# Kernel optimization log

Hardware: AMD Instinct MI355X
Metric: run time of the kernel (lower is better)

Reference implementation:

```python
import jax, jax.numpy as jnp
import numpy as np

D_IN = 2048
NUM_HEADS = 16
QK_NOPE = 64
QK_ROPE = 64
QK_HEAD = QK_NOPE + QK_ROPE  # 128
V_HEAD = 128
KV_LORA = 1024
SEQ = 4096
BATCH = 1
SCALE = QK_HEAD ** -0.5
EPS = 1e-6


def rmsnorm(x, w):
    return x * jax.lax.rsqrt(jnp.mean(x * x, axis=-1, keepdims=True) + EPS) * w


def apply_rope(x, cos, sin):
    # x: [B, S, H, D]; cos/sin: [S, D//2]; pairs are consecutive elements (view_as_complex)
    b, s, h, d = x.shape
    xr = x.reshape(b, s, h, d // 2, 2)
    xe, xo = xr[..., 0], xr[..., 1]
    c = cos[None, :, None, :]
    sn = sin[None, :, None, :]
    oe = xe * c - xo * sn
    oo = xe * sn + xo * c
    return jnp.stack([oe, oo], axis=-1).reshape(b, s, h, d)


def setup_inputs() -> dict:
    key = jax.random.key(0)
    ks = jax.random.split(key, 8)
    x = jax.random.normal(ks[0], (BATCH, SEQ, D_IN), dtype=jnp.float32)
    # rotary tables (rope_theta=10000)
    inv_freq = 1.0 / (10000.0 ** (np.arange(0, QK_ROPE, 2, dtype=np.float32) / QK_ROPE))
    angles = np.arange(SEQ, dtype=np.float32)[:, None] * inv_freq[None, :]
    cos = jnp.asarray(np.cos(angles), dtype=jnp.float32)
    sin = jnp.asarray(np.sin(angles), dtype=jnp.float32)
    # causal additive mask [S, S]
    mask = jnp.where(jnp.triu(jnp.ones((SEQ, SEQ), dtype=bool), k=1), -1e9, 0.0).astype(jnp.float32)
    def lin(k, fan_out, fan_in):
        bound = 1.0 / np.sqrt(fan_in)
        return jax.random.uniform(k, (fan_out, fan_in), jnp.float32, -bound, bound)
    wq = lin(ks[1], NUM_HEADS * QK_HEAD, D_IN)
    wkv_a = lin(ks[2], KV_LORA + QK_ROPE, D_IN)
    kv_norm_w = jnp.ones((KV_LORA,), dtype=jnp.float32)
    wkv_b = lin(ks[3], NUM_HEADS * (QK_NOPE + V_HEAD), KV_LORA)
    wo = lin(ks[4], D_IN, NUM_HEADS * V_HEAD)
    return {"x": x, "cos": cos, "sin": sin, "mask": mask, "wq": wq,
            "wkv_a": wkv_a, "kv_norm_w": kv_norm_w, "wkv_b": wkv_b, "wo": wo,
            "start_pos": 0}


def reference(x, cos, sin, mask, wq, wkv_a, kv_norm_w, wkv_b, wo, start_pos):
    b, s, _ = x.shape
    # Q projection -> [B, S, H, qk_head_dim]
    q = (x @ wq.T).reshape(b, s, NUM_HEADS, QK_HEAD)
    q_nope, q_pe = q[..., :QK_NOPE], q[..., QK_NOPE:]
    q_pe = apply_rope(q_pe, cos, sin)
    # KV low-rank projection
    kv_full = x @ wkv_a.T                               # [B, S, KV_LORA + QK_ROPE]
    kv, k_pe = kv_full[..., :KV_LORA], kv_full[..., KV_LORA:]
    k_pe = apply_rope(k_pe[:, :, None, :], cos, sin)    # [B, S, 1, QK_ROPE]
    # naive path: expand latent to per-head k_nope / v
    q = jnp.concatenate([q_nope, q_pe], axis=-1)        # [B, S, H, 128]
    kvb = (rmsnorm(kv, kv_norm_w) @ wkv_b.T).reshape(b, s, NUM_HEADS, QK_NOPE + V_HEAD)
    k_nope, v = kvb[..., :QK_NOPE], kvb[..., QK_NOPE:]
    k = jnp.concatenate([k_nope, jnp.broadcast_to(k_pe, (b, s, NUM_HEADS, QK_ROPE))], axis=-1)
    # start_pos=0 prefill: cache[:, :end_pos] == freshly written k, v
    scores = jnp.einsum('bqhd,bkhd->bqhk', q, k) * SCALE  # [B, S, H, S]
    scores = scores + mask[None, :, None, :]
    probs = jax.nn.softmax(scores.astype(jnp.float32), axis=-1).astype(x.dtype)
    out = jnp.einsum('bqhk,bkhd->bqhd', probs, v)       # [B, S, H, V_HEAD]
    return out.reshape(b, s, NUM_HEADS * V_HEAD) @ wo.T
```

## Files before the change

kernel.cpp:

```cpp
#include <hip/hip_runtime.h>

typedef __bf16 bf16;
typedef __attribute__((ext_vector_type(8))) __bf16 bf16x8;
typedef __attribute__((ext_vector_type(2))) __bf16 bf16x2;
typedef __attribute__((ext_vector_type(4))) float f32x4;
typedef __attribute__((ext_vector_type(4))) int int4v;

typedef __attribute__((address_space(1))) const void gconst_t;
typedef __attribute__((address_space(3))) void lvoid_t;

#define SEQ 4096
#define D_IN 2048
#define NHEADS 16
#define QSCALE (0.08838834764831843f * 1.4426950408889634f)
#define RMS_EPS 1e-6f
#define QKV_N 3136

__device__ inline unsigned pack2bf(float a, float b) {
    bf16x2 t; t[0] = (bf16)a; t[1] = (bf16)b;
    return __builtin_bit_cast(unsigned, t);
}

__device__ inline void conv_seg(const float* __restrict__ in, bf16* __restrict__ out,
                                int n, int i0, int stride) {
    for (int i = i0; i < n; i += stride) {
        float4 v = *reinterpret_cast<const float4*>(in + i);
        bf16 o[4];
        o[0] = (bf16)v.x; o[1] = (bf16)v.y; o[2] = (bf16)v.z; o[3] = (bf16)v.w;
        *reinterpret_cast<uint2*>(out + i) = *reinterpret_cast<uint2*>(o);
    }
}

__global__ __launch_bounds__(256) void convert_all_kernel(
    const float* __restrict__ xs,  const float* __restrict__ wqs,
    const float* __restrict__ was, const float* __restrict__ wbs,
    const float* __restrict__ wos,
    bf16* __restrict__ xd, bf16* __restrict__ wqd, bf16* __restrict__ wad,
    bf16* __restrict__ wbd, bf16* __restrict__ wod) {
    int i0 = (blockIdx.x * 256 + threadIdx.x) * 4;
    int stride = gridDim.x * 256 * 4;
    conv_seg(xs,  xd,  4096 * 2048, i0, stride);
    conv_seg(wqs, wqd, 2048 * 2048, i0, stride);
    conv_seg(was, wad, 1088 * 2048, i0, stride);
    conv_seg(wbs, wbd, 3072 * 1024, i0, stride);
    conv_seg(wos, wod, 2048 * 2048, i0, stride);
}

template<int BN, bool BF16_OUT>
__global__ __launch_bounds__(512, 2) void gemm256_kernel(
    const bf16* __restrict__ A, const bf16* __restrict__ B, void* __restrict__ Cout,
    int M, int N, int K) {
    constexpr int CB = BN / 64;
    constexpr int NF = BN / 64;
    constexpr int WC = BN / 4;
    __shared__ __align__(16) bf16 Al[2][256 * 64];
    __shared__ __align__(16) bf16 Bl[2][BN * 64];

    int t    = threadIdx.x;
    int lane = t & 63;
    int w    = t >> 6;
    int wr   = w >> 2;
    int wc   = w & 3;
    int l15  = lane & 15;
    int g    = lane >> 4;
    int m0 = blockIdx.y * 256;
    int n0 = blockIdx.x * BN;

    f32x4 acc[8][NF] = {};

    auto stage = [&](int kt, int buf) {
        int k0 = kt << 6;
        #pragma unroll
        for (int c = 0; c < 4; c++) {
            int idx = c * 512 + t;
            int r = idx >> 3;
            int u = (idx & 7) ^ (r & 7);
            const bf16* ga = A + (size_t)(m0 + r) * K + k0 + u * 8;
            __builtin_amdgcn_global_load_lds((gconst_t*)ga,
                (lvoid_t*)&Al[buf][(c * 512 + w * 64) * 8], 16, 0, 0);
        }
        #pragma unroll
        for (int c = 0; c < CB; c++) {
            int idx = c * 512 + t;
            int r = idx >> 3;
            int u = (idx & 7) ^ (r & 7);
            int br = n0 + r; if (br >= N) br = N - 1;
            const bf16* gb = B + (size_t)br * K + k0 + u * 8;
            __builtin_amdgcn_global_load_lds((gconst_t*)gb,
                (lvoid_t*)&Bl[buf][(c * 512 + w * 64) * 8], 16, 0, 0);
        }
    };

    int nt = K >> 6;
    stage(0, 0);
    for (int kt = 0; kt < nt; ++kt) {
        int buf = kt & 1;
        if (kt + 1 < nt) {
            stage(kt + 1, buf ^ 1);
            __builtin_amdgcn_sched_barrier(0);
            if constexpr (BN == 256) asm volatile("s_waitcnt vmcnt(8)" ::: "memory");
            else                     asm volatile("s_waitcnt vmcnt(6)" ::: "memory");
            __builtin_amdgcn_sched_barrier(0);
        } else {
            __builtin_amdgcn_sched_barrier(0);
            asm volatile("s_waitcnt vmcnt(0)" ::: "memory");
            __builtin_amdgcn_sched_barrier(0);
        }
        __builtin_amdgcn_s_barrier();

        #pragma unroll
        for (int ks = 0; ks < 2; ++ks) {
            bf16x8 af[8], bfv[NF];
            #pragma unroll
            for (int mt = 0; mt < 8; mt++) {
                int ra = wr * 128 + mt * 16 + l15;
                int u = (ks * 4 + g) ^ (ra & 7);
                af[mt] = *reinterpret_cast<const bf16x8*>(&Al[buf][ra * 64 + u * 8]);
            }
            #pragma unroll
            for (int nf = 0; nf < NF; nf++) {
                int rb = wc * WC + nf * 16 + l15;
                int u = (ks * 4 + g) ^ (rb & 7);
                bfv[nf] = *reinterpret_cast<const bf16x8*>(&Bl[buf][rb * 64 + u * 8]);
            }
            __builtin_amdgcn_s_setprio(1);
            #pragma unroll
            for (int mt = 0; mt < 8; mt++)
                #pragma unroll
                for (int nf = 0; nf < NF; nf++)
                    acc[mt][nf] = __builtin_amdgcn_mfma_f32_16x16x32_bf16(af[mt], bfv[nf], acc[mt][nf], 0, 0, 0);
            __builtin_amdgcn_s_setprio(0);
        }
        __builtin_amdgcn_s_barrier();
    }

    #pragma unroll
    for (int mt = 0; mt < 8; mt++) {
        #pragma unroll
        for (int nf = 0; nf < NF; nf++) {
            int col = n0 + wc * WC + nf * 16 + l15;
            if (col < N) {
                #pragma unroll
                for (int r = 0; r < 4; r++) {
                    int row = m0 + wr * 128 + mt * 16 + g * 4 + r;
                    if (BF16_OUT)
                        ((bf16*)Cout)[(size_t)row * N + col] = (bf16)acc[mt][nf][r];
                    else
                        ((float*)Cout)[(size_t)row * N + col] = acc[mt][nf][r];
                }
            }
        }
    }
}

__global__ __launch_bounds__(256) void prep_qkv_kernel(
    bf16* __restrict__ qkv, const float* __restrict__ w,
    const float* __restrict__ cosb, const float* __restrict__ sinb,
    bf16* __restrict__ kvnorm, bf16* __restrict__ kpe) {
    __shared__ float red[4];
    int s = blockIdx.x;
    int t = threadIdx.x;

    const bf16* src = qkv + (size_t)s * QKV_N + 2048;
    float f[4];
    {
        uint2 raw = *reinterpret_cast<const uint2*>(src + t * 4);
        bf16* vb = reinterpret_cast<bf16*>(&raw);
        float ss = 0.f;
        #pragma unroll
        for (int j = 0; j < 4; j++) { f[j] = (float)vb[j]; ss += f[j] * f[j]; }
        #pragma unroll
        for (int m = 1; m < 64; m <<= 1) ss += __shfl_xor(ss, m);
        if ((t & 63) == 0) red[t >> 6] = ss;
    }
    __syncthreads();
    float tot = red[0] + red[1] + red[2] + red[3];
    float rms = rsqrtf(tot * (1.0f / 1024.0f) + RMS_EPS);
    bf16 o[4];
    #pragma unroll
    for (int j = 0; j < 4; j++) o[j] = (bf16)(f[j] * rms * w[t*4 + j]);
    *reinterpret_cast<uint2*>(kvnorm + (size_t)s * 1024 + t * 4) = *reinterpret_cast<uint2*>(o);
    if (t < 16) {
        float e[4];
        #pragma unroll
        for (int j = 0; j < 4; j++) e[j] = (float)src[1024 + t*4 + j];
        int ib = t * 2;
        float c0 = cosb[s*32 + ib],     s0 = sinb[s*32 + ib];
        float c1 = cosb[s*32 + ib + 1], s1 = sinb[s*32 + ib + 1];
        bf16 ko[4];
        ko[0] = (bf16)(e[0]*c0 - e[1]*s0);
        ko[1] = (bf16)(e[0]*s0 + e[1]*c0);
        ko[2] = (bf16)(e[2]*c1 - e[3]*s1);
        ko[3] = (bf16)(e[2]*s1 + e[3]*c1);
        *reinterpret_cast<uint2*>(kpe + (size_t)s * 64 + t * 4) = *reinterpret_cast<uint2*>(ko);
    }

    bf16* p = qkv + (size_t)s * QKV_N + t * 8;
    bf16x8 v = *reinterpret_cast<bf16x8*>(p);
    float qf[8];
    #pragma unroll
    for (int j = 0; j < 8; j++) qf[j] = (float)v[j];
    int d0 = (t & 15) * 8;
    if (d0 >= 64) {
        int ib = (d0 - 64) >> 1;
        #pragma unroll
        for (int pr = 0; pr < 4; pr++) {
            float c  = cosb[s * 32 + ib + pr];
            float sn = sinb[s * 32 + ib + pr];
            float xe = qf[pr*2], xo = qf[pr*2 + 1];
            qf[pr*2]     = xe * c - xo * sn;
            qf[pr*2 + 1] = xe * sn + xo * c;
        }
    }
    #pragma unroll
    for (int j = 0; j < 8; j++) v[j] = (bf16)(qf[j] * QSCALE);
    *reinterpret_cast<bf16x8*>(p) = v;
}

__global__ __launch_bounds__(256) void build_vt_kernel(
    const bf16* __restrict__ kvb, bf16* __restrict__ vt) {
    const int LT = 130;
    __shared__ bf16 lt[64 * 130];
    int h  = blockIdx.y;
    int s0 = blockIdx.x * 64;
    int t  = threadIdx.x;
    {
        int row = t >> 2;
        int d0  = (t & 3) * 32;
        const bf16* src = kvb + (size_t)(s0 + row) * 3072 + h * 192 + 64 + d0;
        int4v v0 = *reinterpret_cast<const int4v*>(src);
        int4v v1 = *reinterpret_cast<const int4v*>(src + 8);
        int4v v2 = *reinterpret_cast<const int4v*>(src + 16);
        int4v v3 = *reinterpret_cast<const int4v*>(src + 24);
        int* dst = reinterpret_cast<int*>(&lt[row * LT + d0]);
        int* s0p = reinterpret_cast<int*>(&v0); int* s1p = reinterpret_cast<int*>(&v1);
        int* s2p = reinterpret_cast<int*>(&v2); int* s3p = reinterpret_cast<int*>(&v3);
        #pragma unroll
        for (int j = 0; j < 4; j++) { dst[j] = s0p[j]; dst[4+j] = s1p[j]; dst[8+j] = s2p[j]; dst[12+j] = s3p[j]; }
    }
    __syncthreads();
    int ss = t & 63;
    int db = t >> 6;
    bf16* out = vt + (size_t)h * 128 * 4096 + s0 + ss;
    #pragma unroll
    for (int dd = db; dd < 128; dd += 4)
        out[(size_t)dd * 4096] = lt[ss * LT + dd];
}

__global__ __launch_bounds__(256, 2) void attn_kernel(
    const bf16* __restrict__ q,
    const bf16* __restrict__ kvb,
    const bf16* __restrict__ kpe,
    const bf16* __restrict__ vt,
    bf16* __restrict__ attn) {
    const int LPS = 72;
    __shared__ __align__(16) bf16 Kl[2][64 * 128];
    __shared__ __align__(16) bf16 Vl[2][128 * 64];
    __shared__ __align__(16) bf16 Pl[4][16 * 72];
    __shared__ __align__(16) float bcast[4][16];

    int h    = blockIdx.y;
    int tile = (h < 8) ? (31 - (int)blockIdx.x) : (int)blockIdx.x;
    int q0   = tile * 128;
    int t  = threadIdx.x;
    int lane = t & 63;
    int w  = t >> 6;
    int l15 = lane & 15;
    int g   = lane >> 4;
    int sw  = l15 & 7;
    int qrow = q0 + w * 32;

    const bf16* kvbh = kvb + h * 192;
    const bf16* vth  = vt + (size_t)h * 524288;

    bf16x8 qf[2][4];
    #pragma unroll
    for (int mt = 0; mt < 2; mt++) {
        const bf16* qp = q + (size_t)(qrow + mt*16 + l15) * QKV_N + h * 128 + g * 8;
        #pragma unroll
        for (int c = 0; c < 4; c++) qf[mt][c] = *reinterpret_cast<const bf16x8*>(qp + c * 32);
    }

    f32x4 o[2][8] = {};
    float mrow[2], lrow[2];
    #pragma unroll
    for (int mt = 0; mt < 2; mt++) { mrow[mt] = -3e38f; lrow[mt] = 0.f; }

    int nch = (q0 >> 6) + 2;
    int dc  = (q0 >> 6) + (w >> 1);

    auto stageK = [&](int jc, int buf) {
        int j0 = jc << 6;
        #pragma unroll
        for (int c = 0; c < 4; c++) {
            int idx = c*256 + w*64 + lane;
            int row = idx >> 4;
            int u   = (idx & 15) ^ (row & 7);
            const bf16* src = (u < 8)
                ? kvbh + (size_t)(j0 + row) * 3072 + u * 8
                : kpe  + (size_t)(j0 + row) * 64  + (u - 8) * 8;
            __builtin_amdgcn_global_load_lds((gconst_t*)src,
                (lvoid_t*)&Kl[buf][(c*256 + w*64) * 8], 16, 0, 0);
        }
    };
    auto stageV = [&](int jc, int buf) {
        int j0 = jc << 6;
        #pragma unroll
        for (int c = 0; c < 4; c++) {
            int idx = c*256 + w*64 + lane;
            int row = idx >> 3;
            int u   = (idx & 7) ^ (row & 7);
            const bf16* src = vth + (size_t)row * 4096 + j0 + u * 8;
            __builtin_amdgcn_global_load_lds((gconst_t*)src,
                (lvoid_t*)&Vl[buf][(c*256 + w*64) * 8], 16, 0, 0);
        }
    };

    stageK(0, 0); stageV(0, 0);

    for (int jc = 0; jc < nch; ++jc) {
        __syncthreads();
        if (jc + 1 < nch) { stageK(jc + 1, (jc + 1) & 1); stageV(jc + 1, (jc + 1) & 1); }

        if (jc <= dc) {
            int cur = jc & 1;
            int j0  = jc << 6;
            bool masked = (jc == dc);

            f32x4 sfr[2][4];
            #pragma unroll
            for (int s = 0; s < 4; ++s) {
                int krow = s*16 + l15;
                bf16x8 kf[4];
                #pragma unroll
                for (int c = 0; c < 4; ++c)
                    kf[c] = *reinterpret_cast<const bf16x8*>(
                        &Kl[cur][krow*128 + (((c*4 + g) ^ sw) * 8)]);
                #pragma unroll
                for (int mt = 0; mt < 2; ++mt) {
                    f32x4 acc = {};
                    acc = __builtin_amdgcn_mfma_f32_16x16x32_bf16(kf[0], qf[mt][0], acc, 0, 0, 0);
                    acc = __builtin_amdgcn_mfma_f32_16x16x32_bf16(kf[1], qf[mt][1], acc, 0, 0, 0);
                    acc = __builtin_amdgcn_mfma_f32_16x16x32_bf16(kf[2], qf[mt][2], acc, 0, 0, 0);
                    acc = __builtin_amdgcn_mfma_f32_16x16x32_bf16(kf[3], qf[mt][3], acc, 0, 0, 0);
                    sfr[mt][s] = acc;
                }
            }

            bf16x8 pf[2][2];
            #pragma unroll
            for (int mt = 0; mt < 2; ++mt) {
                int i = qrow + mt*16 + l15;
                if (masked) {
                    #pragma unroll
                    for (int s = 0; s < 4; ++s)
                        #pragma unroll
                        for (int r = 0; r < 4; ++r) {
                            int j = j0 + s*16 + g*4 + r;
                            if (j > i) sfr[mt][s][r] = -3e38f;
                        }
                }
                float m01 = fmaxf(fmaxf(sfr[mt][0][0], sfr[mt][0][1]),
                                  fmaxf(sfr[mt][0][2], sfr[mt][0][3]));
                float m23 = fmaxf(fmaxf(sfr[mt][1][0], sfr[mt][1][1]),
                                  fmaxf(sfr[mt][1][2], sfr[mt][1][3]));
                float m45 = fmaxf(fmaxf(sfr[mt][2][0], sfr[mt][2][1]),
                                  fmaxf(sfr[mt][2][2], sfr[mt][2][3]));
                float m67 = fmaxf(fmaxf(sfr[mt][3][0], sfr[mt][3][1]),
                                  fmaxf(sfr[mt][3][2], sfr[mt][3][3]));
                float mloc = fmaxf(fmaxf(m01, m23), fmaxf(m45, m67));
                float mx = fmaxf(mloc, __shfl_xor(mloc, 16));
                mx = fmaxf(mx, __shfl_xor(mx, 32));
                bool need = mx > mrow[mt];
                float mnew = fmaxf(mrow[mt], mx);
                float sfac = __builtin_amdgcn_exp2f(mrow[mt] - mnew);
                mrow[mt] = mnew;
                float psum = 0.f;
                #pragma unroll
                for (int s = 0; s < 4; ++s)
                    #pragma unroll
                    for (int r = 0; r < 4; ++r) {
                        float p = __builtin_amdgcn_exp2f(sfr[mt][s][r] - mnew);
                        sfr[mt][s][r] = p;
                        psum += p;
                    }
                lrow[mt] = lrow[mt] * sfac + psum;
                #pragma unroll
                for (int s = 0; s < 4; ++s) {
                    unsigned u0 = pack2bf(sfr[mt][s][0], sfr[mt][s][1]);
                    unsigned u1 = pack2bf(sfr[mt][s][2], sfr[mt][s][3]);
                    *reinterpret_cast<unsigned*>(&Pl[w][l15 * LPS + s*16 + g*4])     = u0;
                    *reinterpret_cast<unsigned*>(&Pl[w][l15 * LPS + s*16 + g*4 + 2]) = u1;
                }
                if (g == 0) bcast[w][l15] = sfac;
                f32x4 sf4 = *reinterpret_cast<const f32x4*>(&bcast[w][g*4]);
                if (__any(need)) {
                    #pragma unroll
                    for (int dt = 0; dt < 8; ++dt)
                        #pragma unroll
                        for (int r = 0; r < 4; ++r) o[mt][dt][r] *= sf4[r];
                }
                pf[mt][0] = *reinterpret_cast<const bf16x8*>(&Pl[w][l15 * LPS + g * 8]);
                pf[mt][1] = *reinterpret_cast<const bf16x8*>(&Pl[w][l15 * LPS + 32 + g * 8]);
            }

            #pragma unroll
            for (int dt = 0; dt < 8; ++dt) {
                int vrow = dt*16 + l15;
                bf16x8 va = *reinterpret_cast<const bf16x8*>(
                    &Vl[cur][vrow*64 + ((g ^ sw) * 8)]);
                bf16x8 vb = *reinterpret_cast<const bf16x8*>(
                    &Vl[cur][vrow*64 + (((4 + g) ^ sw) * 8)]);
                o[0][dt] = __builtin_amdgcn_mfma_f32_16x16x32_bf16(pf[0][0], va, o[0][dt], 0, 0, 0);
                o[0][dt] = __builtin_amdgcn_mfma_f32_16x16x32_bf16(pf[0][1], vb, o[0][dt], 0, 0, 0);
                o[1][dt] = __builtin_amdgcn_mfma_f32_16x16x32_bf16(pf[1][0], va, o[1][dt], 0, 0, 0);
                o[1][dt] = __builtin_amdgcn_mfma_f32_16x16x32_bf16(pf[1][1], vb, o[1][dt], 0, 0, 0);
            }
        }
    }

    #pragma unroll
    for (int mt = 0; mt < 2; ++mt) {
        float l = lrow[mt];
        l += __shfl_xor(l, 16);
        l += __shfl_xor(l, 32);
        float linv = __builtin_amdgcn_rcpf(l);
        if (g == 0) bcast[w][l15] = linv;
        f32x4 li4 = *reinterpret_cast<const f32x4*>(&bcast[w][g*4]);
        #pragma unroll
        for (int r = 0; r < 4; ++r) {
            int i = qrow + mt*16 + g*4 + r;
            #pragma unroll
            for (int dt = 0; dt < 8; ++dt)
                attn[(size_t)i * 2048 + h * 128 + dt*16 + l15] = (bf16)(o[mt][dt][r] * li4[r]);
        }
    }
}

extern "C" void kernel_launch(void* const* d_in, const int* in_sizes, int n_in,
                              void* d_out, int out_size, void* d_ws, size_t ws_size,
                              hipStream_t stream) {
    const float* x    = (const float*)d_in[0];
    const float* cosb = (const float*)d_in[1];
    const float* sinb = (const float*)d_in[2];
    const float* wq   = (const float*)d_in[4];
    const float* wkva = (const float*)d_in[5];
    const float* kvw  = (const float*)d_in[6];
    const float* wkvb = (const float*)d_in[7];
    const float* wo   = (const float*)d_in[8];

    char* ws = (char*)d_ws;
    bf16* x_bf    = (bf16*)(ws + 0);
    bf16* kvnorm  = (bf16*)(ws + 0);
    bf16* attn    = (bf16*)(ws + 0);
    bf16* wq_bf   = (bf16*)(ws + 16777216);
    bf16* wkva_bf = (bf16*)(ws + 25165824);
    bf16* wkvb_bf = (bf16*)(ws + 29622272);
    bf16* wo_bf   = (bf16*)(ws + 35913728);
    bf16* qkv     = (bf16*)(ws + 44302336);
    bf16* kpe     = (bf16*)(ws + 69992448);
    bf16* kvb     = (bf16*)(ws + 70516736);
    bf16* vt      = (bf16*)(ws + 95682560);

    convert_all_kernel<<<dim3(2048), dim3(256), 0, stream>>>(
        x, wq, wkva, wkvb, wo, x_bf, wq_bf, wkva_bf, wkvb_bf, wo_bf);

    gemm256_kernel<256, true><<<dim3(13, 16), dim3(512), 0, stream>>>(x_bf, wq_bf, qkv, 4096, QKV_N, 2048);

    prep_qkv_kernel<<<dim3(4096), dim3(256), 0, stream>>>(qkv, kvw, cosb, sinb, kvnorm, kpe);

    gemm256_kernel<256, true><<<dim3(12, 16), dim3(512), 0, stream>>>(kvnorm, wkvb_bf, kvb, 4096, 3072, 1024);

    build_vt_kernel<<<dim3(64, 16), dim3(256), 0, stream>>>(kvb, vt);

    attn_kernel<<<dim3(32, 16), dim3(256), 0, stream>>>(qkv, kvb, kpe, vt, attn);

    gemm256_kernel<128, false><<<dim3(16, 16), dim3(512), 0, stream>>>(attn, wo_bf, (float*)d_out, 4096, 2048, 2048);
}
```

Measured before the change: 327.7 us.

## Shrink attention query tile to 64 rows and drop K/V double buffering

The attention kernel now handles 64 query rows per block (16 per wave) instead of 128, launches twice as many blocks, and uses single-buffered K/V shared memory with load-then-sync instead of a prefetched double buffer. Occupancy rises to 3 blocks per CU thanks to the smaller LDS and register footprint. The aim is more parallelism and better load balance across the causal triangle. In exchange, each K/V chunk is loaded twice as often per query row, there is no overlap between loads and compute inside a block, and MFMA reuse of each K fragment is halved.

```diff
diff --git a/kernel.cpp b/kernel.cpp
--- a/kernel.cpp
+++ b/kernel.cpp
@@ -247,49 +247,45 @@
         out[(size_t)dd * 4096] = lt[ss * LT + dd];
 }
 
-__global__ __launch_bounds__(256, 2) void attn_kernel(
+__global__ __launch_bounds__(256, 3) void attn_kernel(
     const bf16* __restrict__ q,
     const bf16* __restrict__ kvb,
     const bf16* __restrict__ kpe,
     const bf16* __restrict__ vt,
     bf16* __restrict__ attn) {
     const int LPS = 72;
-    __shared__ __align__(16) bf16 Kl[2][64 * 128];
-    __shared__ __align__(16) bf16 Vl[2][128 * 64];
+    __shared__ __align__(16) bf16 Kl[64 * 128];
+    __shared__ __align__(16) bf16 Vl[128 * 64];
     __shared__ __align__(16) bf16 Pl[4][16 * 72];
     __shared__ __align__(16) float bcast[4][16];
 
     int h    = blockIdx.y;
-    int tile = (h < 8) ? (31 - (int)blockIdx.x) : (int)blockIdx.x;
-    int q0   = tile * 128;
+    int tile = 63 - (int)blockIdx.x;
+    int q0   = tile * 64;
     int t  = threadIdx.x;
     int lane = t & 63;
     int w  = t >> 6;
     int l15 = lane & 15;
     int g   = lane >> 4;
     int sw  = l15 & 7;
-    int qrow = q0 + w * 32;
+    int qrow = q0 + w * 16;
 
     const bf16* kvbh = kvb + h * 192;
     const bf16* vth  = vt + (size_t)h * 524288;
 
-    bf16x8 qf[2][4];
-    #pragma unroll
-    for (int mt = 0; mt < 2; mt++) {
-        const bf16* qp = q + (size_t)(qrow + mt*16 + l15) * QKV_N + h * 128 + g * 8;
-        #pragma unroll
-        for (int c = 0; c < 4; c++) qf[mt][c] = *reinterpret_cast<const bf16x8*>(qp + c * 32);
-    }
-
-    f32x4 o[2][8] = {};
-    float mrow[2], lrow[2];
-    #pragma unroll
-    for (int mt = 0; mt < 2; mt++) { mrow[mt] = -3e38f; lrow[mt] = 0.f; }
-
-    int nch = (q0 >> 6) + 2;
-    int dc  = (q0 >> 6) + (w >> 1);
-
-    auto stageK = [&](int jc, int buf) {
+    bf16x8 qf[4];
+    {
+        const bf16* qp = q + (size_t)(qrow + l15) * QKV_N + h * 128 + g * 8;
+        #pragma unroll
+        for (int c = 0; c < 4; c++) qf[c] = *reinterpret_cast<const bf16x8*>(qp + c * 32);
+    }
+
+    f32x4 o[8] = {};
+    float mrow = -3e38f, lrow = 0.f;
+
+    int nch = tile + 1;
+
+    auto stageK = [&](int jc) {
         int j0 = jc << 6;
         #pragma unroll
         for (int c = 0; c < 4; c++) {
@@ -300,10 +296,10 @@
                 ? kvbh + (size_t)(j0 + row) * 3072 + u * 8
                 : kpe  + (size_t)(j0 + row) * 64  + (u - 8) * 8;
             __builtin_amdgcn_global_load_lds((gconst_t*)src,
-                (lvoid_t*)&Kl[buf][(c*256 + w*64) * 8], 16, 0, 0);
+                (lvoid_t*)&Kl[(c*256 + w*64) * 8], 16, 0, 0);
         }
     };
-    auto stageV = [&](int jc, int buf) {
+    auto stageV = [&](int jc) {
         int j0 = jc << 6;
         #pragma unroll
         for (int c = 0; c < 4; c++) {
@@ -312,116 +308,97 @@
             int u   = (idx & 7) ^ (row & 7);
             const bf16* src = vth + (size_t)row * 4096 + j0 + u * 8;
             __builtin_amdgcn_global_load_lds((gconst_t*)src,
-                (lvoid_t*)&Vl[buf][(c*256 + w*64) * 8], 16, 0, 0);
+                (lvoid_t*)&Vl[(c*256 + w*64) * 8], 16, 0, 0);
         }
     };
 
-    stageK(0, 0); stageV(0, 0);
-
     for (int jc = 0; jc < nch; ++jc) {
+        stageK(jc); stageV(jc);
         __syncthreads();
-        if (jc + 1 < nch) { stageK(jc + 1, (jc + 1) & 1); stageV(jc + 1, (jc + 1) & 1); }
-
-        if (jc <= dc) {
-            int cur = jc & 1;
-            int j0  = jc << 6;
-            bool masked = (jc == dc);
-
-            f32x4 sfr[2][4];
-            #pragma unroll
-            for (int s = 0; s < 4; ++s) {
-                int krow = s*16 + l15;
-                bf16x8 kf[4];
+        int j0 = jc << 6;
+        bool masked = (jc == tile);
+
+        f32x4 sfr[4];
+        #pragma unroll
+        for (int s = 0; s < 4; ++s) {
+            int krow = s*16 + l15;
+            bf16x8 kf[4];
+            #pragma unroll
+            for (int c = 0; c < 4; ++c)
+                kf[c] = *reinterpret_cast<const bf16x8*>(
+                    &Kl[krow*128 + (((c*4 + g) ^ sw) * 8)]);
+            f32x4 acc = {};
+            acc = __builtin_amdgcn_mfma_f32_16x16x32_bf16(kf[0], qf[0], acc, 0, 0, 0);
+            acc = __builtin_amdgcn_mfma_f32_16x16x32_bf16(kf[1], qf[1], acc, 0, 0, 0);
+            acc = __builtin_amdgcn_mfma_f32_16x16x32_bf16(kf[2], qf[2], acc, 0, 0, 0);
+            acc = __builtin_amdgcn_mfma_f32_16x16x32_bf16(kf[3], qf[3], acc, 0, 0, 0);
+            sfr[s] = acc;
+        }
+
+        int i = qrow + l15;
+        if (masked) {
+            #pragma unroll
+            for (int s = 0; s < 4; ++s)
                 #pragma unroll
-                for (int c = 0; c < 4; ++c)
-                    kf[c] = *reinterpret_cast<const bf16x8*>(
-                        &Kl[cur][krow*128 + (((c*4 + g) ^ sw) * 8)]);
+                for (int r = 0; r < 4; ++r) {
+                    int j = j0 + s*16 + g*4 + r;
+                    if (j > i) sfr[s][r] = -3e38f;
+                }
+        }
+        float m01 = fmaxf(fmaxf(sfr[0][0], sfr[0][1]), fmaxf(sfr[0][2], sfr[0][3]));
+        float m23 = fmaxf(fmaxf(sfr[1][0], sfr[1][1]), fmaxf(sfr[1][2], sfr[1][3]));
+        float m45 = fmaxf(fmaxf(sfr[2][0], sfr[2][1]), fmaxf(sfr[2][2], sfr[2][3]));
+        float m67 = fmaxf(fmaxf(sfr[3][0], sfr[3][1]), fmaxf(sfr[3][2], sfr[3][3]));
+        float mloc = fmaxf(fmaxf(m01, m23), fmaxf(m45, m67));
+        float mx = fmaxf(mloc, __shfl_xor(mloc, 16));
+        mx = fmaxf(mx, __shfl_xor(mx, 32));
+        bool need = mx > mrow;
+        float mnew = fmaxf(mrow, mx);
+        float sfac = __builtin_amdgcn_exp2f(mrow - mnew);
+        mrow = mnew;
+        float psum = 0.f;
+        #pragma unroll
+        for (int s = 0; s < 4; ++s)
+            #pragma unroll
+            for (int r = 0; r < 4; ++r) {
+                float p = __builtin_amdgcn_exp2f(sfr[s][r] - mnew);
+                sfr[s][r] = p;
+                psum += p;
+            }
+        lrow = lrow * sfac + psum;
+        #pragma unroll
+        for (int s = 0; s < 4; ++s) {
+            unsigned u0 = pack2bf(sfr[s][0], sfr[s][1]);
+            unsigned u1 = pack2bf(sfr[s][2], sfr[s][3]);
+            *reinterpret_cast<unsigned*>(&Pl[w][l15 * LPS + s*16 + g*4])     = u0;
+            *reinterpret_cast<unsigned*>(&Pl[w][l15 * LPS + s*16 + g*4 + 2]) = u1;
+        }
+        if (g == 0) bcast[w][l15] = sfac;
+        f32x4 sf4 = *reinterpret_cast<const f32x4*>(&bcast[w][g*4]);
+        if (__any(need)) {
+            #pragma unroll
+            for (int dt = 0; dt < 8; ++dt)
                 #pragma unroll
-                for (int mt = 0; mt < 2; ++mt) {
-                    f32x4 acc = {};
-                    acc = __builtin_amdgcn_mfma_f32_16x16x32_bf16(kf[0], qf[mt][0], acc, 0, 0, 0);
-                    acc = __builtin_amdgcn_mfma_f32_16x16x32_bf16(kf[1], qf[mt][1], acc, 0, 0, 0);
-                    acc = __builtin_amdgcn_mfma_f32_16x16x32_bf16(kf[2], qf[mt][2], acc, 0, 0, 0);
-                    acc = __builtin_amdgcn_mfma_f32_16x16x32_bf16(kf[3], qf[mt][3], acc, 0, 0, 0);
-                    sfr[mt][s] = acc;
-                }
-            }
-
-            bf16x8 pf[2][2];
-            #pragma unroll
-            for (int mt = 0; mt < 2; ++mt) {
-                int i = qrow + mt*16 + l15;
-                if (masked) {
-                    #pragma unroll
-                    for (int s = 0; s < 4; ++s)
-                        #pragma unroll
-                        for (int r = 0; r < 4; ++r) {
-                            int j = j0 + s*16 + g*4 + r;
-                            if (j > i) sfr[mt][s][r] = -3e38f;
-                        }
-                }
-                float m01 = fmaxf(fmaxf(sfr[mt][0][0], sfr[mt][0][1]),
-                                  fmaxf(sfr[mt][0][2], sfr[mt][0][3]));
-                float m23 = fmaxf(fmaxf(sfr[mt][1][0], sfr[mt][1][1]),
-                                  fmaxf(sfr[mt][1][2], sfr[mt][1][3]));
-                float m45 = fmaxf(fmaxf(sfr[mt][2][0], sfr[mt][2][1]),
-                                  fmaxf(sfr[mt][2][2], sfr[mt][2][3]));
-                float m67 = fmaxf(fmaxf(sfr[mt][3][0], sfr[mt][3][1]),
-                                  fmaxf(sfr[mt][3][2], sfr[mt][3][3]));
-                float mloc = fmaxf(fmaxf(m01, m23), fmaxf(m45, m67));
-                float mx = fmaxf(mloc, __shfl_xor(mloc, 16));
-                mx = fmaxf(mx, __shfl_xor(mx, 32));
-                bool need = mx > mrow[mt];
-                float mnew = fmaxf(mrow[mt], mx);
-                float sfac = __builtin_amdgcn_exp2f(mrow[mt] - mnew);
-                mrow[mt] = mnew;
-                float psum = 0.f;
-                #pragma unroll
-                for (int s = 0; s < 4; ++s)
-                    #pragma unroll
-                    for (int r = 0; r < 4; ++r) {
-                        float p = __builtin_amdgcn_exp2f(sfr[mt][s][r] - mnew);
-                        sfr[mt][s][r] = p;
-                        psum += p;
-                    }
-                lrow[mt] = lrow[mt] * sfac + psum;
-                #pragma unroll
-                for (int s = 0; s < 4; ++s) {
-                    unsigned u0 = pack2bf(sfr[mt][s][0], sfr[mt][s][1]);
-                    unsigned u1 = pack2bf(sfr[mt][s][2], sfr[mt][s][3]);
-                    *reinterpret_cast<unsigned*>(&Pl[w][l15 * LPS + s*16 + g*4])     = u0;
-                    *reinterpret_cast<unsigned*>(&Pl[w][l15 * LPS + s*16 + g*4 + 2]) = u1;
-                }
-                if (g == 0) bcast[w][l15] = sfac;
-                f32x4 sf4 = *reinterpret_cast<const f32x4*>(&bcast[w][g*4]);
-                if (__any(need)) {
-                    #pragma unroll
-                    for (int dt = 0; dt < 8; ++dt)
-                        #pragma unroll
-                        for (int r = 0; r < 4; ++r) o[mt][dt][r] *= sf4[r];
-                }
-                pf[mt][0] = *reinterpret_cast<const bf16x8*>(&Pl[w][l15 * LPS + g * 8]);
-                pf[mt][1] = *reinterpret_cast<const bf16x8*>(&Pl[w][l15 * LPS + 32 + g * 8]);
-            }
-
-            #pragma unroll
-            for (int dt = 0; dt < 8; ++dt) {
-                int vrow = dt*16 + l15;
-                bf16x8 va = *reinterpret_cast<const bf16x8*>(
-                    &Vl[cur][vrow*64 + ((g ^ sw) * 8)]);
-                bf16x8 vb = *reinterpret_cast<const bf16x8*>(
-                    &Vl[cur][vrow*64 + (((4 + g) ^ sw) * 8)]);
-                o[0][dt] = __builtin_amdgcn_mfma_f32_16x16x32_bf16(pf[0][0], va, o[0][dt], 0, 0, 0);
-                o[0][dt] = __builtin_amdgcn_mfma_f32_16x16x32_bf16(pf[0][1], vb, o[0][dt], 0, 0, 0);
-                o[1][dt] = __builtin_amdgcn_mfma_f32_16x16x32_bf16(pf[1][0], va, o[1][dt], 0, 0, 0);
-                o[1][dt] = __builtin_amdgcn_mfma_f32_16x16x32_bf16(pf[1][1], vb, o[1][dt], 0, 0, 0);
-            }
-        }
-    }
-
-    #pragma unroll
-    for (int mt = 0; mt < 2; ++mt) {
-        float l = lrow[mt];
+                for (int r = 0; r < 4; ++r) o[dt][r] *= sf4[r];
+        }
+        bf16x8 pf0 = *reinterpret_cast<const bf16x8*>(&Pl[w][l15 * LPS + g * 8]);
+        bf16x8 pf1 = *reinterpret_cast<const bf16x8*>(&Pl[w][l15 * LPS + 32 + g * 8]);
+
+        #pragma unroll
+        for (int dt = 0; dt < 8; ++dt) {
+            int vrow = dt*16 + l15;
+            bf16x8 va = *reinterpret_cast<const bf16x8*>(
+                &Vl[vrow*64 + ((g ^ sw) * 8)]);
+            bf16x8 vb = *reinterpret_cast<const bf16x8*>(
+                &Vl[vrow*64 + (((4 + g) ^ sw) * 8)]);
+            o[dt] = __builtin_amdgcn_mfma_f32_16x16x32_bf16(pf0, va, o[dt], 0, 0, 0);
+            o[dt] = __builtin_amdgcn_mfma_f32_16x16x32_bf16(pf1, vb, o[dt], 0, 0, 0);
+        }
+        __syncthreads();
+    }
+
+    {
+        float l = lrow;
         l += __shfl_xor(l, 16);
         l += __shfl_xor(l, 32);
         float linv = __builtin_amdgcn_rcpf(l);
@@ -429,10 +406,10 @@
         f32x4 li4 = *reinterpret_cast<const f32x4*>(&bcast[w][g*4]);
         #pragma unroll
         for (int r = 0; r < 4; ++r) {
-            int i = qrow + mt*16 + g*4 + r;
+            int i = qrow + g*4 + r;
             #pragma unroll
             for (int dt = 0; dt < 8; ++dt)
-                attn[(size_t)i * 2048 + h * 128 + dt*16 + l15] = (bf16)(o[mt][dt][r] * li4[r]);
+                attn[(size_t)i * 2048 + h * 128 + dt*16 + l15] = (bf16)(o[dt][r] * li4[r]);
         }
     }
 }
@@ -473,7 +450,7 @@
 
     build_vt_kernel<<<dim3(64, 16), dim3(256), 0, stream>>>(kvb, vt);
 
-    attn_kernel<<<dim3(32, 16), dim3(256), 0, stream>>>(qkv, kvb, kpe, vt, attn);
+    attn_kernel<<<dim3(64, 16), dim3(256), 0, stream>>>(qkv, kvb, kpe, vt, attn);
 
     gemm256_kernel<128, false><<<dim3(16, 16), dim3(512), 0, stream>>>(attn, wo_bf, (float*)d_out, 4096, 2048, 2048);
 }
```

Measured after the change: 371.6 us. +13.4%, slower.

## Interleave next-tile global-to-LDS loads across four compute phases in GEMM

Applied to the files above, without the earlier changes.

The GEMM K-loop is split into four phases, each covering half a K-step and half the M rows. The global_load_lds prefetches for the next tile are spread across these phases instead of being issued all at once, so memory traffic overlaps MFMA work more evenly. Only four A fragments are held at a time, which lowers register pressure. In exchange there are more workgroup barriers per K tile, and a tighter vmcnt wait at phase 0.

```diff
diff --git a/kernel.cpp b/kernel.cpp
--- a/kernel.cpp
+++ b/kernel.cpp
@@ -68,70 +68,75 @@
 
     f32x4 acc[8][NF] = {};
 
-    auto stage = [&](int kt, int buf) {
-        int k0 = kt << 6;
-        #pragma unroll
-        for (int c = 0; c < 4; c++) {
-            int idx = c * 512 + t;
-            int r = idx >> 3;
-            int u = (idx & 7) ^ (r & 7);
-            const bf16* ga = A + (size_t)(m0 + r) * K + k0 + u * 8;
-            __builtin_amdgcn_global_load_lds((gconst_t*)ga,
-                (lvoid_t*)&Al[buf][(c * 512 + w * 64) * 8], 16, 0, 0);
-        }
-        #pragma unroll
-        for (int c = 0; c < CB; c++) {
-            int idx = c * 512 + t;
-            int r = idx >> 3;
-            int u = (idx & 7) ^ (r & 7);
-            int br = n0 + r; if (br >= N) br = N - 1;
-            const bf16* gb = B + (size_t)br * K + k0 + u * 8;
-            __builtin_amdgcn_global_load_lds((gconst_t*)gb,
-                (lvoid_t*)&Bl[buf][(c * 512 + w * 64) * 8], 16, 0, 0);
-        }
+    auto stageA = [&](int kt2, int buf2, int c) {
+        int k0 = kt2 << 6;
+        int idx = c * 512 + t;
+        int r = idx >> 3;
+        int u = (idx & 7) ^ (r & 7);
+        const bf16* ga = A + (size_t)(m0 + r) * K + k0 + u * 8;
+        __builtin_amdgcn_global_load_lds((gconst_t*)ga,
+            (lvoid_t*)&Al[buf2][(c * 512 + w * 64) * 8], 16, 0, 0);
     };
+    auto stageB = [&](int kt2, int buf2, int c) {
+        int k0 = kt2 << 6;
+        int idx = c * 512 + t;
+        int r = idx >> 3;
+        int u = (idx & 7) ^ (r & 7);
+        int br = n0 + r; if (br >= N) br = N - 1;
+        const bf16* gb = B + (size_t)br * K + k0 + u * 8;
+        __builtin_amdgcn_global_load_lds((gconst_t*)gb,
+            (lvoid_t*)&Bl[buf2][(c * 512 + w * 64) * 8], 16, 0, 0);
+    };
 
     int nt = K >> 6;
-    stage(0, 0);
+    #pragma unroll
+    for (int c = 0; c < 4; c++)  stageA(0, 0, c);
+    #pragma unroll
+    for (int c = 0; c < CB; c++) stageB(0, 0, c);
+
     for (int kt = 0; kt < nt; ++kt) {
         int buf = kt & 1;
-        if (kt + 1 < nt) {
-            stage(kt + 1, buf ^ 1);
-            __builtin_amdgcn_sched_barrier(0);
-            if constexpr (BN == 256) asm volatile("s_waitcnt vmcnt(8)" ::: "memory");
-            else                     asm volatile("s_waitcnt vmcnt(6)" ::: "memory");
-            __builtin_amdgcn_sched_barrier(0);
-        } else {
-            __builtin_amdgcn_sched_barrier(0);
-            asm volatile("s_waitcnt vmcnt(0)" ::: "memory");
-            __builtin_amdgcn_sched_barrier(0);
-        }
-        __builtin_amdgcn_s_barrier();
-
-        #pragma unroll
-        for (int ks = 0; ks < 2; ++ks) {
-            bf16x8 af[8], bfv[NF];
-            #pragma unroll
-            for (int mt = 0; mt < 8; mt++) {
-                int ra = wr * 128 + mt * 16 + l15;
+        bool has_next = (kt + 1 < nt);
+        bf16x8 bfv[NF];
+        #pragma unroll
+        for (int ph = 0; ph < 4; ++ph) {
+            int ks = ph >> 1, mh = ph & 1;
+            if (has_next) {
+                stageA(kt + 1, buf ^ 1, ph);
+                if (ph < CB) stageB(kt + 1, buf ^ 1, ph);
+            }
+            if (ph == 0) {
+                __builtin_amdgcn_sched_barrier(0);
+                if (has_next) asm volatile("s_waitcnt vmcnt(2)" ::: "memory");
+                else          asm volatile("s_waitcnt vmcnt(0)" ::: "memory");
+                __builtin_amdgcn_sched_barrier(0);
+            }
+            __builtin_amdgcn_s_barrier();
+            bf16x8 af4[4];
+            #pragma unroll
+            for (int j = 0; j < 4; j++) {
+                int ra = wr * 128 + (mh * 4 + j) * 16 + l15;
                 int u = (ks * 4 + g) ^ (ra & 7);
-                af[mt] = *reinterpret_cast<const bf16x8*>(&Al[buf][ra * 64 + u * 8]);
-            }
-            #pragma unroll
-            for (int nf = 0; nf < NF; nf++) {
-                int rb = wc * WC + nf * 16 + l15;
-                int u = (ks * 4 + g) ^ (rb & 7);
-                bfv[nf] = *reinterpret_cast<const bf16x8*>(&Bl[buf][rb * 64 + u * 8]);
+                af4[j] = *reinterpret_cast<const bf16x8*>(&Al[buf][ra * 64 + u * 8]);
+            }
+            if (mh == 0) {
+                #pragma unroll
+                for (int nf = 0; nf < NF; nf++) {
+                    int rb = wc * WC + nf * 16 + l15;
+                    int u = (ks * 4 + g) ^ (rb & 7);
+                    bfv[nf] = *reinterpret_cast<const bf16x8*>(&Bl[buf][rb * 64 + u * 8]);
+                }
             }
             __builtin_amdgcn_s_setprio(1);
             #pragma unroll
-            for (int mt = 0; mt < 8; mt++)
+            for (int j = 0; j < 4; j++)
                 #pragma unroll
                 for (int nf = 0; nf < NF; nf++)
-                    acc[mt][nf] = __builtin_amdgcn_mfma_f32_16x16x32_bf16(af[mt], bfv[nf], acc[mt][nf], 0, 0, 0);
+                    acc[mh * 4 + j][nf] = __builtin_amdgcn_mfma_f32_16x16x32_bf16(
+                        af4[j], bfv[nf], acc[mh * 4 + j][nf], 0, 0, 0);
             __builtin_amdgcn_s_setprio(0);
-        }
-        __builtin_amdgcn_s_barrier();
+            __builtin_amdgcn_s_barrier();
+        }
     }
 
     #pragma unroll
```

Measured after the change: 391.0 us. +19.3%, slower.
